# Optimization experiments

Hardware: AMD Instinct MI355X
Metric: run time of the kernel (lower is better)

The kernel has to match this reference:

```python
import jax, jax.numpy as jnp
import numpy as np

# dims
B = 2
HC, WC = 96, 96      # coarse spatial
HF, WF = 384, 384
CIN_C = 256          # in_coarser_channels
CIN_F = 3            # in_finer_channels
CH = 64              # hidden_channels
COUT = 19            # out_channels
KS, DIL = 3, 1       # local attention window


def conv2d(x, w, b=None, pad=0):
    y = jax.lax.conv_general_dilated(
        x, w, window_strides=(1, 1), padding=[(pad, pad), (pad, pad)],
        dimension_numbers=("NCHW", "OIHW", "NCHW"))
    if b is not None:
        y = y + b[None, :, None, None]
    return y


def upsample_nearest(x, factor):
    return jnp.repeat(jnp.repeat(x, factor, axis=2), factor, axis=3)


def local_attn_2d(q, k, v, kernel_size=KS, dilation=DIL):
    # per-pixel attention over a (kernel_size x kernel_size) dilated neighborhood
    Bq, C, H, W = q.shape
    Cv = v.shape[1]
    pad = dilation * (kernel_size - 1) // 2
    kp = jnp.pad(k, ((0, 0), (0, 0), (pad, pad), (pad, pad)))
    vp = jnp.pad(v, ((0, 0), (0, 0), (pad, pad), (pad, pad)))
    offs = [(i * dilation, j * dilation)
            for i in range(kernel_size) for j in range(kernel_size)]
    # scores: (B, K*K, H, W) -- q . k_neighbor per offset (zero-padded borders)
    scores = jnp.stack(
        [(q * kp[:, :, oi:oi + H, oj:oj + W]).sum(axis=1) for oi, oj in offs],
        axis=1)
    attn = jax.nn.softmax(scores, axis=1)
    y = jnp.zeros((Bq, Cv, H, W), q.dtype)
    for idx, (oi, oj) in enumerate(offs):
        y = y + attn[:, idx:idx + 1] * vp[:, :, oi:oi + H, oj:oj + W]
    return y


def setup_inputs() -> dict:
    key = jax.random.key(0)
    ks = jax.random.split(key, 11)
    p = lambda i, shape: jax.random.normal(ks[i], shape, jnp.float32) * 0.05
    return dict(
        coarse_feature=jax.random.normal(ks[0], (B, CIN_C, HC, WC), jnp.float32),
        raw_image=jax.random.uniform(ks[1], (B, CIN_F, HF, WF), jnp.float32),
        w_ef=p(2, (1, CIN_F, 3, 3)), b_ef=p(3, (1,)),          # edge_finer conv3x3
        w_ec=p(4, (CH, CIN_C, 3, 3)), b_ec=p(5, (CH,)),        # edge_coarser conv3x3
        w_eh=p(6, (1, CH + 1, 1, 1)),                          # edge_head conv1x1, no bias
        w_q=p(7, (CH, CIN_F, 1, 1)), b_q=p(8, (CH,)),          # xq_head conv1x1
        w_v=p(9, (COUT, CIN_C + CH, 1, 1)), b_v=p(10, (COUT,)) # xv_head conv1x1
    )


def reference(coarse_feature, raw_image, w_ef, b_ef, w_ec, b_ec, w_eh,
              w_q, b_q, w_v, b_v):
    f = HF // HC
    # edge branch
    ef = jax.nn.relu(conv2d(raw_image, w_ef, b_ef, pad=1))           # (B,1,HF,WF)
    ec = jax.nn.relu(conv2d(coarse_feature, w_ec, b_ec, pad=1))      # (B,CH,HC,WC)
    edge_logit = conv2d(jnp.concatenate([upsample_nearest(ec, f), ef], axis=1), w_eh)
    non_edge = jax.nn.sigmoid(edge_logit)                            # (B,1,HF,WF)
    # q / k / v
    xq = conv2d(raw_image, w_q, b_q)                                 # (B,CH,HF,WF)
    xk = non_edge * xq
    xv = conv2d(jnp.concatenate([upsample_nearest(coarse_feature, f), xq], axis=1),
                w_v, b_v)                                            # (B,COUT,HF,WF)
    y = local_attn_2d(xq, xk, xv)
    return y, non_edge
```

## Files before the change

kernel.cpp:

```cpp
#include <hip/hip_runtime.h>
#include <math.h>

#define B_    2
#define HC_   96
#define WC_   96
#define HF_   384
#define WF_   384
#define CINC_ 256
#define CH_   64
#define COUT_ 19

typedef __attribute__((ext_vector_type(8))) short bf16x8;
typedef __attribute__((ext_vector_type(4))) float f32x4;

__device__ __forceinline__ unsigned short f2bf(float f) {
    unsigned int u = __float_as_uint(f);
    u += 0x7fffu + ((u >> 16) & 1u);
    return (unsigned short)(u >> 16);
}
__device__ __forceinline__ unsigned int pk2(float a, float b) {
    return (unsigned int)f2bf(a) | ((unsigned int)f2bf(b) << 16);
}
__device__ __forceinline__ float bflo(unsigned int u) { return __uint_as_float(u << 16); }
__device__ __forceinline__ float bfhi(unsigned int u) { return __uint_as_float(u & 0xffff0000u); }

__device__ __forceinline__ void gl_lds16(const void* g, void* l) {
    __builtin_amdgcn_global_load_lds(
        (const __attribute__((address_space(1))) void*)g,
        (__attribute__((address_space(3))) void*)l, 16, 0, 0);
}

__global__ __launch_bounds__(256) void k_pre(
    const float* __restrict__ x,
    const float* __restrict__ w_ec, const float* __restrict__ w_v,
    const float* __restrict__ w_q,  const float* __restrict__ b_q,
    const float* __restrict__ b_v,
    unsigned short* __restrict__ Xt,
    unsigned short* __restrict__ A_pk, unsigned short* __restrict__ Avc,
    float* __restrict__ drv)
{
    const int bid = blockIdx.x;
    const int tid = threadIdx.x;
    if (bid < 576) {
        int i = bid * 256 + tid;
        {
            int e = i & 7, l = (i >> 3) & 63, m = (i >> 9) & 3, ck = (i >> 11) & 7, tap = i >> 14;
            int oc = m * 16 + (l & 15);
            int ch = ck * 32 + (l >> 4) * 8 + e;
            A_pk[i] = f2bf(w_ec[(oc * 256 + ch) * 9 + tap]);
        }
        if (i < 8192) {
            int e = i & 7, l = (i >> 3) & 63, m = (i >> 9) & 1, ck = (i >> 10) & 7;
            int ov = m * 16 + (l & 15);
            int ch = ck * 32 + (l >> 4) * 8 + e;
            Avc[i] = (ov < COUT_) ? f2bf(w_v[ov * 320 + ch]) : (unsigned short)0;
        }
        return;
    }
    if (bid < 580) {
        int e = (bid - 576) * 256 + tid;
        if (e >= 388 * B_) return;
        int b = e / 388, i = e - b * 388;
        int gy, gx;
        if (i < 98)       { gy = 0;           gx = i; }
        else if (i < 196) { gy = 97;          gx = i - 98; }
        else if (i < 292) { gy = i - 196 + 1; gx = 0; }
        else              { gy = i - 292 + 1; gx = 97; }
        uint4* dst = (uint4*)(Xt + (((size_t)(b * 98 + gy)) * 98 + gx) * 256);
        uint4 zz; zz.x = zz.y = zz.z = zz.w = 0u;
        #pragma unroll
        for (int c = 0; c < 32; ++c) dst[c] = zz;
        return;
    }
    if (bid < 1156) {
        int u = bid - 580;
        int bx = u % 36;
        int rb = u / 36;
        int b  = rb & 1;
        int cz = (rb >> 1) * 32;
        int px = bx * 256 + tid;
        int gy = px / 96, gx = px - gy * 96;
        const float* src = x + (size_t)b * CINC_ * 9216;
        unsigned short* dst = Xt + (((size_t)(b * 98 + gy + 1)) * 98 + gx + 1) * 256;
        for (int c0 = cz; c0 < cz + 32; c0 += 8) {
            float f[8];
            #pragma unroll
            for (int t = 0; t < 8; ++t) f[t] = src[(size_t)(c0 + t) * 9216 + px];
            uint4 v;
            v.x = pk2(f[0], f[1]);
            v.y = pk2(f[2], f[3]);
            v.z = pk2(f[4], f[5]);
            v.w = pk2(f[6], f[7]);
            *(uint4*)&dst[c0] = v;
        }
        return;
    }
    {
        int i = tid;
        if (i < 9) {
            int ci = i / 3, cj = i % 3;
            float a = 0.f;
            for (int c = 0; c < 64; ++c) a += w_q[c * 3 + ci] * w_q[c * 3 + cj];
            drv[i] = a;
        } else if (i < 12) {
            int ci = i - 9;
            float a = 0.f;
            for (int c = 0; c < 64; ++c) a += w_q[c * 3 + ci] * b_q[c];
            drv[i] = a;
        } else if (i == 12) {
            float a = 0.f;
            for (int c = 0; c < 64; ++c) a += b_q[c] * b_q[c];
            drv[12] = a;
        } else if (i < 70) {
            int idx = i - 13, ci = idx / 19, ov = idx % 19;
            float a = 0.f;
            for (int c = 0; c < 64; ++c) a += w_v[ov * 320 + 256 + c] * w_q[c * 3 + ci];
            drv[i] = a;
        } else if (i < 89) {
            int ov = i - 70;
            float a = b_v[ov];
            for (int c = 0; c < 64; ++c) a += w_v[ov * 320 + 256 + c] * b_q[c];
            drv[i] = a;
        }
        return;
    }
}

__global__ __launch_bounds__(256, 2) void k_ec(
    const unsigned short* __restrict__ Xt,
    const unsigned short* __restrict__ A_pk,
    const unsigned short* __restrict__ Avc,
    const float* __restrict__ b_ec, const float* __restrict__ w_eh,
    float* __restrict__ eh4,
    float* __restrict__ cvb)
{
    __shared__ uint4 sB[2][768];

    const int tid  = threadIdx.x;
    const int lane = tid & 63;
    const int wv   = tid >> 6;
    const int j    = lane & 15;
    const int g    = lane >> 4;
    const int zb   = blockIdx.z;
    const int z    = zb & 3;
    const int b    = zb >> 2;
    const int ty0  = blockIdx.y * 8;
    const int tx0  = blockIdx.x * 16;

    f32x4 acc0 = (f32x4)0.f, acc1 = (f32x4)0.f;
    f32x4 accv[2][2];
    accv[0][0] = accv[0][1] = accv[1][0] = accv[1][1] = (f32x4)0.f;

    const bf16x8* Af  = (const bf16x8*)A_pk;
    const bf16x8* Avf = (const bf16x8*)Avc;

#define STAGE_EC(BUF, CK)                                                      \
    {                                                                          \
        _Pragma("unroll")                                                      \
        for (int rr = 0; rr < 3; ++rr) {                                       \
            int slot = 192 * wv + 64 * rr + lane;                              \
            int px = slot >> 2;                                                \
            px = px > 179 ? 179 : px;                                          \
            int part = (slot & 3) ^ ((px >> 1) & 3);                           \
            int row = px / 18, col = px - row * 18;                            \
            const unsigned short* src = Xt                                     \
                + (((size_t)(b * 98 + ty0 + row)) * 98 + (tx0 + col)) * 256    \
                + (CK) * 32 + part * 8;                                        \
            gl_lds16(src, &sB[BUF][192 * wv + 64 * rr]);                       \
        }                                                                      \
    }

    STAGE_EC(0, 0);
    __syncthreads();

    for (int ck = 0; ck < 8; ++ck) {
        const int cur = ck & 1;
        if (ck < 7) STAGE_EC(cur ^ 1, ck + 1);

        bf16x8 frg[4][3];
        #pragma unroll
        for (int rr = 0; rr < 4; ++rr)
            #pragma unroll
            for (int dx = 0; dx < 3; ++dx) {
                int px = (2 * wv + rr) * 18 + j + dx;
                int slot = (px << 2) + (g ^ ((px >> 1) & 3));
                frg[rr][dx] = *(const bf16x8*)&sB[cur][slot];
            }

        #pragma unroll
        for (int tap = 0; tap < 9; ++tap) {
            const int dy = tap / 3, dx = tap % 3;
            bf16x8 a = Af[((tap * 8 + ck) * 4 + z) * 64 + lane];
            acc0 = __builtin_amdgcn_mfma_f32_16x16x32_bf16(a, frg[dy][dx], acc0, 0, 0, 0);
            acc1 = __builtin_amdgcn_mfma_f32_16x16x32_bf16(a, frg[dy + 1][dx], acc1, 0, 0, 0);
        }
        if (z == 0) {
            bf16x8 av0 = Avf[(ck * 2 + 0) * 64 + lane];
            bf16x8 av1 = Avf[(ck * 2 + 1) * 64 + lane];
            accv[0][0] = __builtin_amdgcn_mfma_f32_16x16x32_bf16(av0, frg[1][1], accv[0][0], 0, 0, 0);
            accv[0][1] = __builtin_amdgcn_mfma_f32_16x16x32_bf16(av0, frg[2][1], accv[0][1], 0, 0, 0);
            accv[1][0] = __builtin_amdgcn_mfma_f32_16x16x32_bf16(av1, frg[1][1], accv[1][0], 0, 0, 0);
            accv[1][1] = __builtin_amdgcn_mfma_f32_16x16x32_bf16(av1, frg[2][1], accv[1][1], 0, 0, 0);
        }
        if (ck < 7) __syncthreads();
    }
#undef STAGE_EC

    float we[4], be[4];
    #pragma unroll
    for (int q = 0; q < 4; ++q) {
        int oc = z * 16 + 4 * g + q;
        we[q] = w_eh[oc];
        be[q] = b_ec[oc];
    }
    #pragma unroll
    for (int r = 0; r < 2; ++r) {
        const f32x4 accr = r ? acc1 : acc0;
        float p = 0.f;
        #pragma unroll
        for (int q = 0; q < 4; ++q)
            p += we[q] * fmaxf(accr[q] + be[q], 0.f);
        p += __shfl_xor(p, 16);
        p += __shfl_xor(p, 32);
        const int gpix = (ty0 + 2 * wv + r) * WC_ + tx0 + j;
        if (g == 0)
            eh4[((size_t)b * (HC_ * WC_) + gpix) * 4 + z] = p;
        if (z == 0) {
            float* cvp = cvb + ((size_t)b * (HC_ * WC_) + gpix) * 20;
            #pragma unroll
            for (int m = 0; m < 2; ++m)
                #pragma unroll
                for (int q = 0; q < 4; ++q) {
                    int ov = m * 16 + 4 * g + q;
                    if (ov < 20) cvp[ov] = accv[m][r][q];
                }
        }
    }
}

__global__ __launch_bounds__(256, 4) void k_fine(
    const float* __restrict__ raw,
    const float* __restrict__ w_ef, const float* __restrict__ b_ef,
    const float* __restrict__ w_eh,
    const float* __restrict__ drv,
    const float* __restrict__ eh4,
    const float* __restrict__ cvb,
    float* __restrict__ out_y,
    float* __restrict__ out_ne)
{
    __shared__ float sRaw[3][20][20];
    __shared__ unsigned short sV[324 * 26];
    __shared__ float sNE[324];

    const int tid = threadIdx.x;
    const int b   = blockIdx.z;
    const int ty0 = blockIdx.y * 16;
    const int tx0 = blockIdx.x * 16;
    const float* rb = raw + (size_t)b * 3 * (HF_ * WF_);

    const float* Gm = drv;
    const float* uv = drv + 9;
    const float* Mm = drv + 13;
    const float* bc = drv + 70;

    for (int i = tid; i < 1200; i += 256) {
        int ch = i / 400, rem = i - ch * 400;
        int ry = rem / 20, rx = rem - ry * 20;
        int gh = ty0 + ry - 2, gw = tx0 + rx - 2;
        float v = 0.f;
        if (gh >= 0 && gh < HF_ && gw >= 0 && gw < WF_)
            v = rb[(size_t)ch * (HF_ * WF_) + gh * WF_ + gw];
        sRaw[ch][ry][rx] = v;
    }
    __syncthreads();

    for (int p = tid; p < 324; p += 256) {
        const int iy = p / 18, ix = p - iy * 18;
        const int gh = ty0 + iy - 1, gw = tx0 + ix - 1;
        unsigned int* vw = (unsigned int*)&sV[p * 26];
        if (gh < 0 || gh >= HF_ || gw < 0 || gw >= WF_) {
            #pragma unroll
            for (int w = 0; w < 10; ++w) vw[w] = 0u;
            sNE[p] = 0.f;
            continue;
        }
        float ef = b_ef[0];
        #pragma unroll
        for (int ci = 0; ci < 3; ++ci)
            #pragma unroll
            for (int t = 0; t < 9; ++t)
                ef = fmaf(w_ef[ci * 9 + t], sRaw[ci][iy + t / 3][ix + t % 3], ef);
        ef = fmaxf(ef, 0.f);

        const int cpix = (gh >> 2) * WC_ + (gw >> 2);
        const float4 ehv = *(const float4*)(eh4 + ((size_t)b * (HC_ * WC_) + cpix) * 4);
        float logit = fmaf(w_eh[64], ef, (ehv.x + ehv.y) + (ehv.z + ehv.w));
        float ne = 1.f / (1.f + __expf(-logit));
        sNE[p] = ne;

        const float r0 = sRaw[0][iy + 1][ix + 1];
        const float r1 = sRaw[1][iy + 1][ix + 1];
        const float r2 = sRaw[2][iy + 1][ix + 1];

        float v[20];
        {
            const float4* cvp = (const float4*)(cvb + ((size_t)b * (HC_ * WC_) + cpix) * 20);
            float4 c0 = cvp[0], c1 = cvp[1], c2 = cvp[2], c3 = cvp[3], c4 = cvp[4];
            v[0] = c0.x; v[1] = c0.y; v[2] = c0.z; v[3] = c0.w;
            v[4] = c1.x; v[5] = c1.y; v[6] = c1.z; v[7] = c1.w;
            v[8] = c2.x; v[9] = c2.y; v[10] = c2.z; v[11] = c2.w;
            v[12] = c3.x; v[13] = c3.y; v[14] = c3.z; v[15] = c3.w;
            v[16] = c4.x; v[17] = c4.y; v[18] = c4.z;
        }
        #pragma unroll
        for (int ov = 0; ov < COUT_; ++ov)
            v[ov] = fmaf(Mm[38 + ov], r2,
                    fmaf(Mm[19 + ov], r1,
                    fmaf(Mm[ov], r0, v[ov] + bc[ov])));

        #pragma unroll
        for (int o2 = 0; o2 < 9; ++o2)
            vw[o2] = pk2(v[2 * o2], v[2 * o2 + 1]);
        vw[9] = (unsigned int)f2bf(v[18]);
    }
    __syncthreads();

    const int py = tid >> 4, px2 = tid & 15;
    const int iy = py + 1, ix = px2 + 1;
    const int pbase = iy * 18 + ix;

    float rn[3][9];
    #pragma unroll
    for (int ci = 0; ci < 3; ++ci)
        #pragma unroll
        for (int k = 0; k < 9; ++k)
            rn[ci][k] = sRaw[ci][iy + k / 3][ix + k % 3];

    const float rc0 = rn[0][4], rc1 = rn[1][4], rc2 = rn[2][4];
    const float h0 = fmaf(Gm[0], rc0, fmaf(Gm[1], rc1, fmaf(Gm[2], rc2, uv[0])));
    const float h1 = fmaf(Gm[3], rc0, fmaf(Gm[4], rc1, fmaf(Gm[5], rc2, uv[1])));
    const float h2 = fmaf(Gm[6], rc0, fmaf(Gm[7], rc1, fmaf(Gm[8], rc2, uv[2])));
    const float ac = fmaf(uv[0], rc0, fmaf(uv[1], rc1, fmaf(uv[2], rc2, drv[12])));

    float sc[9];
    #pragma unroll
    for (int k = 0; k < 9; ++k) {
        float d = fmaf(h0, rn[0][k], fmaf(h1, rn[1][k], fmaf(h2, rn[2][k], ac)));
        const int pn = pbase + (k / 3 - 1) * 18 + (k % 3 - 1);
        sc[k] = sNE[pn] * d;
    }
    float mmax = sc[0];
    #pragma unroll
    for (int k = 1; k < 9; ++k) mmax = fmaxf(mmax, sc[k]);
    float e[9];
    float ssum = 0.f;
    #pragma unroll
    for (int k = 0; k < 9; ++k) { e[k] = __expf(sc[k] - mmax); ssum += e[k]; }
    const float inv = 1.f / ssum;

    float y[COUT_];
    #pragma unroll
    for (int ov = 0; ov < COUT_; ++ov) y[ov] = 0.f;
    #pragma unroll
    for (int k = 0; k < 9; ++k) {
        const int pn = pbase + (k / 3 - 1) * 18 + (k % 3 - 1);
        const float a = e[k] * inv;
        const unsigned int* vp = (const unsigned int*)&sV[pn * 26];
        #pragma unroll
        for (int o2 = 0; o2 < 9; ++o2) {
            unsigned int u = vp[o2];
            y[2 * o2]     = fmaf(a, bflo(u), y[2 * o2]);
            y[2 * o2 + 1] = fmaf(a, bfhi(u), y[2 * o2 + 1]);
        }
        y[18] = fmaf(a, bflo(vp[9]), y[18]);
    }

    const int gh = ty0 + py, gw = tx0 + px2;
    const size_t ppos = (size_t)gh * WF_ + gw;
    #pragma unroll
    for (int ov = 0; ov < COUT_; ++ov)
        out_y[((size_t)b * COUT_ + ov) * (HF_ * WF_) + ppos] = y[ov];
    out_ne[(size_t)b * (HF_ * WF_) + ppos] = sNE[pbase];
}

extern "C" void kernel_launch(void* const* d_in, const int* in_sizes, int n_in,
                              void* d_out, int out_size, void* d_ws, size_t ws_size,
                              hipStream_t stream)
{
    const float* coarse = (const float*)d_in[0];
    const float* raw    = (const float*)d_in[1];
    const float* w_ef   = (const float*)d_in[2];
    const float* b_ef   = (const float*)d_in[3];
    const float* w_ec   = (const float*)d_in[4];
    const float* b_ec   = (const float*)d_in[5];
    const float* w_eh   = (const float*)d_in[6];
    const float* w_q    = (const float*)d_in[7];
    const float* b_q    = (const float*)d_in[8];
    const float* w_v    = (const float*)d_in[9];
    const float* b_v    = (const float*)d_in[10];
    (void)in_sizes; (void)n_in; (void)out_size; (void)ws_size;

    unsigned char* ws = (unsigned char*)d_ws;
    size_t off = 0;
    unsigned short* Xt    = (unsigned short*)(ws + off); off += (size_t)B_ * 98 * 98 * 256 * 2;
    unsigned short* A_pk  = (unsigned short*)(ws + off); off += 294912;
    unsigned short* Avc   = (unsigned short*)(ws + off); off += 16384;
    float* eh4    = (float*)(ws + off); off += (size_t)B_ * 9216 * 4 * 4;
    float* cvb    = (float*)(ws + off); off += (size_t)B_ * 9216 * 20 * 4;
    float* drv    = (float*)(ws + off); off += 512;

    float* out_y  = (float*)d_out;
    float* out_ne = out_y + (size_t)B_ * COUT_ * HF_ * WF_;

    hipLaunchKernelGGL(k_pre, dim3(1157), dim3(256), 0, stream,
                       coarse, w_ec, w_v, w_q, b_q, b_v, Xt, A_pk, Avc, drv);
    hipLaunchKernelGGL(k_ec, dim3(6, 12, 4 * B_), dim3(256), 0, stream,
                       Xt, A_pk, Avc, b_ec, w_eh, eh4, cvb);
    hipLaunchKernelGGL(k_fine, dim3(24, 24, B_), dim3(256), 0, stream,
                       raw, w_ef, b_ef, w_eh, drv, eh4, cvb, out_y, out_ne);
}
```

Baseline: 53.42 us.

## Fuse coarse-feature bf16 transpose into conv kernel and remap blocks across XCDs

Removes the separate pass in k_pre that converted the fp32 NCHW coarse feature into a padded bf16 channels-last buffer. k_ec now loads fp32 channels directly from global memory into registers, handles the halo with bounds checks, converts to bf16 and writes a padded LDS tile, prefetching the next channel chunk during the MFMAs. The grid is flattened, and the four z-slices of each spatial tile are mapped so they land on the same XCD to improve L2 sharing. In exchange, the async global-to-LDS double buffer becomes a single buffer with two barriers per chunk, the fp32 loads are strided and uncoalesced-ish, and register pressure goes up.

Result: slower. 55.57 us (+4.0%).

```diff
diff --git a/kernel.cpp b/kernel.cpp
--- a/kernel.cpp
+++ b/kernel.cpp
@@ -24,18 +24,10 @@
 __device__ __forceinline__ float bflo(unsigned int u) { return __uint_as_float(u << 16); }
 __device__ __forceinline__ float bfhi(unsigned int u) { return __uint_as_float(u & 0xffff0000u); }
 
-__device__ __forceinline__ void gl_lds16(const void* g, void* l) {
-    __builtin_amdgcn_global_load_lds(
-        (const __attribute__((address_space(1))) void*)g,
-        (__attribute__((address_space(3))) void*)l, 16, 0, 0);
-}
-
 __global__ __launch_bounds__(256) void k_pre(
-    const float* __restrict__ x,
     const float* __restrict__ w_ec, const float* __restrict__ w_v,
     const float* __restrict__ w_q,  const float* __restrict__ b_q,
     const float* __restrict__ b_v,
-    unsigned short* __restrict__ Xt,
     unsigned short* __restrict__ A_pk, unsigned short* __restrict__ Avc,
     float* __restrict__ drv)
 {
@@ -54,44 +46,6 @@
             int ov = m * 16 + (l & 15);
             int ch = ck * 32 + (l >> 4) * 8 + e;
             Avc[i] = (ov < COUT_) ? f2bf(w_v[ov * 320 + ch]) : (unsigned short)0;
-        }
-        return;
-    }
-    if (bid < 580) {
-        int e = (bid - 576) * 256 + tid;
-        if (e >= 388 * B_) return;
-        int b = e / 388, i = e - b * 388;
-        int gy, gx;
-        if (i < 98)       { gy = 0;           gx = i; }
-        else if (i < 196) { gy = 97;          gx = i - 98; }
-        else if (i < 292) { gy = i - 196 + 1; gx = 0; }
-        else              { gy = i - 292 + 1; gx = 97; }
-        uint4* dst = (uint4*)(Xt + (((size_t)(b * 98 + gy)) * 98 + gx) * 256);
-        uint4 zz; zz.x = zz.y = zz.z = zz.w = 0u;
-        #pragma unroll
-        for (int c = 0; c < 32; ++c) dst[c] = zz;
-        return;
-    }
-    if (bid < 1156) {
-        int u = bid - 580;
-        int bx = u % 36;
-        int rb = u / 36;
-        int b  = rb & 1;
-        int cz = (rb >> 1) * 32;
-        int px = bx * 256 + tid;
-        int gy = px / 96, gx = px - gy * 96;
-        const float* src = x + (size_t)b * CINC_ * 9216;
-        unsigned short* dst = Xt + (((size_t)(b * 98 + gy + 1)) * 98 + gx + 1) * 256;
-        for (int c0 = cz; c0 < cz + 32; c0 += 8) {
-            float f[8];
-            #pragma unroll
-            for (int t = 0; t < 8; ++t) f[t] = src[(size_t)(c0 + t) * 9216 + px];
-            uint4 v;
-            v.x = pk2(f[0], f[1]);
-            v.y = pk2(f[2], f[3]);
-            v.z = pk2(f[4], f[5]);
-            v.w = pk2(f[6], f[7]);
-            *(uint4*)&dst[c0] = v;
         }
         return;
     }
@@ -127,25 +81,78 @@
 }
 
 __global__ __launch_bounds__(256, 2) void k_ec(
-    const unsigned short* __restrict__ Xt,
+    const float* __restrict__ xg,
     const unsigned short* __restrict__ A_pk,
     const unsigned short* __restrict__ Avc,
     const float* __restrict__ b_ec, const float* __restrict__ w_eh,
     float* __restrict__ eh4,
     float* __restrict__ cvb)
 {
-    __shared__ uint4 sB[2][768];
+    __shared__ unsigned short sB[180 * 40];
 
     const int tid  = threadIdx.x;
     const int lane = tid & 63;
     const int wv   = tid >> 6;
     const int j    = lane & 15;
     const int g    = lane >> 4;
-    const int zb   = blockIdx.z;
-    const int z    = zb & 3;
-    const int b    = zb >> 2;
-    const int ty0  = blockIdx.y * 8;
-    const int tx0  = blockIdx.x * 16;
+
+    const int flat = blockIdx.x;
+    const int xcd  = flat & 7;
+    const int slot = flat >> 3;
+    const int t8   = slot >> 2;
+    const int z    = slot & 3;
+    const int tile = t8 * 8 + xcd;
+    const int b    = tile / 72;
+    const int tl   = tile - b * 72;
+    const int ty0  = (tl / 6) * 8;
+    const int tx0  = (tl % 6) * 16;
+
+    const int pxA = tid >> 1, hA = tid & 1;
+    const int uB  = tid + 256;
+    const bool has1 = uB < 360;
+    const int pxB = uB >> 1, hB = uB & 1;
+
+    const int gyA = ty0 + pxA / 18 - 1, gxA = tx0 + pxA % 18 - 1;
+    const int gyB = ty0 + pxB / 18 - 1, gxB = tx0 + pxB % 18 - 1;
+    const bool okA = (gyA >= 0) & (gyA < HC_) & (gxA >= 0) & (gxA < WC_);
+    const bool okB = has1 & (gyB >= 0) & (gyB < HC_) & (gxB >= 0) & (gxB < WC_);
+    const int pA = gyA * WC_ + gxA;
+    const int pB = gyB * WC_ + gxB;
+    const float* xb = xg + (size_t)b * CINC_ * (HC_ * WC_);
+
+    float fA[16], fB[16];
+
+#define LOADCK(CK)                                                              \
+    {                                                                           \
+        const size_t choff = (size_t)((CK) * 32) * (HC_ * WC_);                 \
+        _Pragma("unroll")                                                       \
+        for (int t = 0; t < 16; ++t)                                            \
+            fA[t] = okA ? xb[choff + (size_t)(hA * 16 + t) * (HC_ * WC_) + pA] : 0.f; \
+        _Pragma("unroll")                                                       \
+        for (int t = 0; t < 16; ++t)                                            \
+            fB[t] = okB ? xb[choff + (size_t)(hB * 16 + t) * (HC_ * WC_) + pB] : 0.f; \
+        asm volatile("" ::: "memory");                                          \
+    }
+
+#define WRITECK()                                                               \
+    {                                                                           \
+        uint4 w0, w1;                                                           \
+        w0.x = pk2(fA[0], fA[1]);   w0.y = pk2(fA[2], fA[3]);                   \
+        w0.z = pk2(fA[4], fA[5]);   w0.w = pk2(fA[6], fA[7]);                   \
+        w1.x = pk2(fA[8], fA[9]);   w1.y = pk2(fA[10], fA[11]);                 \
+        w1.z = pk2(fA[12], fA[13]); w1.w = pk2(fA[14], fA[15]);                 \
+        *(uint4*)&sB[pxA * 40 + hA * 16]     = w0;                              \
+        *(uint4*)&sB[pxA * 40 + hA * 16 + 8] = w1;                              \
+        if (has1) {                                                             \
+            uint4 v0, v1;                                                       \
+            v0.x = pk2(fB[0], fB[1]);   v0.y = pk2(fB[2], fB[3]);               \
+            v0.z = pk2(fB[4], fB[5]);   v0.w = pk2(fB[6], fB[7]);               \
+            v1.x = pk2(fB[8], fB[9]);   v1.y = pk2(fB[10], fB[11]);             \
+            v1.z = pk2(fB[12], fB[13]); v1.w = pk2(fB[14], fB[15]);             \
+            *(uint4*)&sB[pxB * 40 + hB * 16]     = v0;                          \
+            *(uint4*)&sB[pxB * 40 + hB * 16 + 8] = v1;                          \
+        }                                                                       \
+    }
 
     f32x4 acc0 = (f32x4)0.f, acc1 = (f32x4)0.f;
     f32x4 accv[2][2];
@@ -154,38 +161,19 @@
     const bf16x8* Af  = (const bf16x8*)A_pk;
     const bf16x8* Avf = (const bf16x8*)Avc;
 
-#define STAGE_EC(BUF, CK)                                                      \
-    {                                                                          \
-        _Pragma("unroll")                                                      \
-        for (int rr = 0; rr < 3; ++rr) {                                       \
-            int slot = 192 * wv + 64 * rr + lane;                              \
-            int px = slot >> 2;                                                \
-            px = px > 179 ? 179 : px;                                          \
-            int part = (slot & 3) ^ ((px >> 1) & 3);                           \
-            int row = px / 18, col = px - row * 18;                            \
-            const unsigned short* src = Xt                                     \
-                + (((size_t)(b * 98 + ty0 + row)) * 98 + (tx0 + col)) * 256    \
-                + (CK) * 32 + part * 8;                                        \
-            gl_lds16(src, &sB[BUF][192 * wv + 64 * rr]);                       \
-        }                                                                      \
-    }
-
-    STAGE_EC(0, 0);
+    LOADCK(0);
+    WRITECK();
     __syncthreads();
 
     for (int ck = 0; ck < 8; ++ck) {
-        const int cur = ck & 1;
-        if (ck < 7) STAGE_EC(cur ^ 1, ck + 1);
+        if (ck < 7) LOADCK(ck + 1);
 
         bf16x8 frg[4][3];
         #pragma unroll
         for (int rr = 0; rr < 4; ++rr)
             #pragma unroll
-            for (int dx = 0; dx < 3; ++dx) {
-                int px = (2 * wv + rr) * 18 + j + dx;
-                int slot = (px << 2) + (g ^ ((px >> 1) & 3));
-                frg[rr][dx] = *(const bf16x8*)&sB[cur][slot];
-            }
+            for (int dx = 0; dx < 3; ++dx)
+                frg[rr][dx] = *(const bf16x8*)&sB[((2 * wv + rr) * 18 + (j + dx)) * 40 + g * 8];
 
         #pragma unroll
         for (int tap = 0; tap < 9; ++tap) {
@@ -202,9 +190,15 @@
             accv[1][0] = __builtin_amdgcn_mfma_f32_16x16x32_bf16(av1, frg[1][1], accv[1][0], 0, 0, 0);
             accv[1][1] = __builtin_amdgcn_mfma_f32_16x16x32_bf16(av1, frg[2][1], accv[1][1], 0, 0, 0);
         }
-        if (ck < 7) __syncthreads();
-    }
-#undef STAGE_EC
+
+        if (ck < 7) {
+            __syncthreads();
+            WRITECK();
+            __syncthreads();
+        }
+    }
+#undef LOADCK
+#undef WRITECK
 
     float we[4], be[4];
     #pragma unroll
@@ -402,7 +396,6 @@
 
     unsigned char* ws = (unsigned char*)d_ws;
     size_t off = 0;
-    unsigned short* Xt    = (unsigned short*)(ws + off); off += (size_t)B_ * 98 * 98 * 256 * 2;
     unsigned short* A_pk  = (unsigned short*)(ws + off); off += 294912;
     unsigned short* Avc   = (unsigned short*)(ws + off); off += 16384;
     float* eh4    = (float*)(ws + off); off += (size_t)B_ * 9216 * 4 * 4;
@@ -412,10 +405,10 @@
     float* out_y  = (float*)d_out;
     float* out_ne = out_y + (size_t)B_ * COUT_ * HF_ * WF_;
 
-    hipLaunchKernelGGL(k_pre, dim3(1157), dim3(256), 0, stream,
-                       coarse, w_ec, w_v, w_q, b_q, b_v, Xt, A_pk, Avc, drv);
-    hipLaunchKernelGGL(k_ec, dim3(6, 12, 4 * B_), dim3(256), 0, stream,
-                       Xt, A_pk, Avc, b_ec, w_eh, eh4, cvb);
+    hipLaunchKernelGGL(k_pre, dim3(577), dim3(256), 0, stream,
+                       w_ec, w_v, w_q, b_q, b_v, A_pk, Avc, drv);
+    hipLaunchKernelGGL(k_ec, dim3(576), dim3(256), 0, stream,
+                       coarse, A_pk, Avc, b_ec, w_eh, eh4, cvb);
     hipLaunchKernelGGL(k_fine, dim3(24, 24, B_), dim3(256), 0, stream,
                        raw, w_ef, b_ef, w_eh, drv, eh4, cvb, out_y, out_ne);
 }
```
